# Kernel optimization log

Measured on AMD Instinct MI355X. Metric: run time of the kernel, lower is better.

The kernel has to match this reference:

```python
import jax, jax.numpy as jnp
import numpy as np

B, S, H, NH, DH, FF, R, NE, EI, NT = 8, 1024, 768, 12, 64, 3072, 64, 512, 4096, 8
EPS = 1e-5


def layer_norm(x, g, b):
    m = jnp.mean(x, axis=-1, keepdims=True)
    v = jnp.var(x, axis=-1, keepdims=True)
    return (x - m) * jax.lax.rsqrt(v + EPS) * g + b


def adapter_apply(h, node_idx, edge_idx, types, dw, db, uw, ub, temb):
    """Hypergraph adapter: bottleneck down-proj, node->hyperedge mean gather,
    edge-type embedding, hyperedge->node mean scatter, up-proj. vmapped over batch."""
    def one(hb, nb, eb, tb):
        d = jax.nn.gelu(hb @ dw + db)                                  # [S, R]
        m = d[nb]                                                      # [EI, R] gather node feats per incidence
        ones = jnp.ones((EI,), d.dtype)
        esum = jax.ops.segment_sum(m, eb, num_segments=NE)             # [NE, R]
        ecnt = jax.ops.segment_sum(ones, eb, num_segments=NE)
        e = esum / jnp.maximum(ecnt, 1.0)[:, None] + temb[tb]          # hyperedge feats + type emb
        nsum = jax.ops.segment_sum(e[eb], nb, num_segments=S)          # scatter back to nodes
        ncnt = jax.ops.segment_sum(ones, nb, num_segments=S)
        u = nsum / jnp.maximum(ncnt, 1.0)[:, None]                     # [S, R]
        return u @ uw + ub                                             # [S, H]
    return jax.vmap(one)(h, node_idx, edge_idx, types)


def setup_inputs() -> dict:
    key = jax.random.key(0)
    ks = jax.random.split(key, 24)
    std = 0.02
    p = lambda k, shp: jax.random.normal(k, shp, jnp.float32) * std
    inp = {
        'hidden_states': jax.random.normal(ks[0], (B, S, H), jnp.float32),
        'node_idx': jax.random.randint(ks[1], (B, EI), 0, S, jnp.int32),
        'edge_idx': jax.random.randint(ks[2], (B, EI), 0, NE, jnp.int32),
        'edge_types': jax.random.randint(ks[3], (B, NE), 0, NT, jnp.int32),
        'Wq': p(ks[4], (H, H)), 'bq': jnp.zeros((H,), jnp.float32),
        'Wk': p(ks[5], (H, H)), 'bk': jnp.zeros((H,), jnp.float32),
        'Wv': p(ks[6], (H, H)), 'bv': jnp.zeros((H,), jnp.float32),
        'Wo': p(ks[7], (H, H)), 'bo': jnp.zeros((H,), jnp.float32),
        'ln1_g': jnp.ones((H,), jnp.float32), 'ln1_b': jnp.zeros((H,), jnp.float32),
        'a1_dw': p(ks[8], (H, R)), 'a1_db': jnp.zeros((R,), jnp.float32),
        'a1_uw': p(ks[9], (R, H)), 'a1_ub': jnp.zeros((H,), jnp.float32),
        'a1_temb': p(ks[10], (NT, R)),
        'Wi': p(ks[11], (H, FF)), 'bi': jnp.zeros((FF,), jnp.float32),
        'Wd2': p(ks[12], (FF, H)), 'bd2': jnp.zeros((H,), jnp.float32),
        'ln2_g': jnp.ones((H,), jnp.float32), 'ln2_b': jnp.zeros((H,), jnp.float32),
        'a2_dw': p(ks[13], (H, R)), 'a2_db': jnp.zeros((R,), jnp.float32),
        'a2_uw': p(ks[14], (R, H)), 'a2_ub': jnp.zeros((H,), jnp.float32),
        'a2_temb': p(ks[15], (NT, R)),
    }
    return inp


def reference(hidden_states, node_idx, edge_idx, edge_types,
              Wq, bq, Wk, bk, Wv, bv, Wo, bo, ln1_g, ln1_b,
              a1_dw, a1_db, a1_uw, a1_ub, a1_temb,
              Wi, bi, Wd2, bd2, ln2_g, ln2_b,
              a2_dw, a2_db, a2_uw, a2_ub, a2_temb):
    x = hidden_states
    # --- self attention ---
    q = (x @ Wq + bq).reshape(B, S, NH, DH)
    k = (x @ Wk + bk).reshape(B, S, NH, DH)
    v = (x @ Wv + bv).reshape(B, S, NH, DH)
    scores = jnp.einsum('bqhd,bkhd->bhqk', q, k) / jnp.sqrt(jnp.float32(DH))
    probs = jax.nn.softmax(scores, axis=-1)
    ctx = jnp.einsum('bhqk,bkhd->bqhd', probs, v).reshape(B, S, H)
    attn_dense = ctx @ Wo + bo                                         # dropout = identity (eval)
    # --- hypergraph adapter 1 + residual LN ---
    ad1 = adapter_apply(attn_dense, node_idx, edge_idx, edge_types, a1_dw, a1_db, a1_uw, a1_ub, a1_temb)
    attn_out = layer_norm(attn_dense + ad1 + x, ln1_g, ln1_b)
    # --- FFN ---
    inter = jax.nn.gelu(attn_out @ Wi + bi)
    ff = inter @ Wd2 + bd2
    # --- hypergraph adapter 2 + residual LN ---
    ad2 = adapter_apply(ff, node_idx, edge_idx, edge_types, a2_dw, a2_db, a2_uw, a2_ub, a2_temb)
    layer_output = layer_norm(ff + ad2 + attn_out, ln2_g, ln2_b)
    return layer_output
```

## Files before the change

### kernel.cpp

```cpp
#include <hip/hip_runtime.h>

typedef unsigned short u16;
typedef __attribute__((ext_vector_type(8))) short s16x8;
typedef __attribute__((ext_vector_type(4))) float f32x4;
typedef __attribute__((ext_vector_type(4))) unsigned short u16x4;

#define NB 8
#define SS 1024
#define HH 768
#define NHD 12
#define DHD 64
#define FFD 3072
#define RR 64
#define NEC 512
#define EIC 4096

__device__ __forceinline__ float b2f(u16 u){ return __uint_as_float(((unsigned)u)<<16); }
__device__ __forceinline__ u16 f2b(float f){
  unsigned x = __float_as_uint(f);
  return (u16)((x + 0x7fffu + ((x>>16)&1u)) >> 16);
}
__device__ __forceinline__ float gelu_f(float x){
  return 0.5f*x*(1.0f + tanhf(0.79788456080286535588f*(x + 0.044715f*x*x*x)));
}
__device__ __forceinline__ void xcd_swz(int gx, int gy, int& bx, int& by){
  const int nwg = gx*gy;
  const int flat = by*gx + bx;
  const int qch = nwg >> 3, rch = nwg & 7;
  const int xcd = flat & 7, idx = flat >> 3;
  const int swz = (xcd < rch ? xcd*(qch+1) : rch*(qch+1) + (xcd-rch)*qch) + idx;
  bx = swz % gx; by = swz / gx;
}

__global__ __launch_bounds__(256)
void cvt16(const float* __restrict__ src, u16* __restrict__ dst)
{
  const size_t i = ((size_t)blockIdx.x*256 + threadIdx.x)*8;
  float4 a = *(const float4*)&src[i];
  float4 b = *(const float4*)&src[i+4];
  u16x4 h1; h1.x=f2b(a.x); h1.y=f2b(a.y); h1.z=f2b(a.z); h1.w=f2b(a.w);
  u16x4 h2; h2.x=f2b(b.x); h2.y=f2b(b.y); h2.z=f2b(b.z); h2.w=f2b(b.w);
  *(u16x4*)&dst[i] = h1; *(u16x4*)&dst[i+4] = h2;
}

__global__ __launch_bounds__(256)
void wtrans(const float* __restrict__ src, u16* __restrict__ dst, int R, int C)
{
  __shared__ u16 tile[64][68];
  const int r0 = blockIdx.x*64, c0 = blockIdx.y*64;
  const int t = threadIdx.x;
  const int tr = t >> 4, tc = (t & 15) * 4;
  for (int i = 0; i < 4; i++) {
    int r = tr + i*16;
    float4 v4 = *(const float4*)&src[(size_t)(r0+r)*C + c0 + tc];
    u16x4 h; h.x = f2b(v4.x); h.y = f2b(v4.y); h.z = f2b(v4.z); h.w = f2b(v4.w);
    *(u16x4*)&tile[r][tc] = h;
  }
  __syncthreads();
  for (int i = 0; i < 4; i++) {
    int rr = tr + i*16;
    u16x4 v;
    v.x = tile[tc+0][rr]; v.y = tile[tc+1][rr];
    v.z = tile[tc+2][rr]; v.w = tile[tc+3][rr];
    *(u16x4*)&dst[(size_t)(c0+rr)*R + r0 + tc] = v;
  }
}

__global__ __launch_bounds__(256)
void vtrans(const u16* __restrict__ v, u16* __restrict__ vt, int vs)
{
  __shared__ u16 tile[64][68];
  const int st = blockIdx.x, bh = blockIdx.y;
  const int b = bh / NHD, h = bh - b*NHD;
  const u16* src = v + (size_t)(b*SS + st*64)*vs + h*DHD;
  u16* dst = vt + (size_t)bh*DHD*SS + st*64;
  const int t = threadIdx.x;
  const int tr = t >> 4, tc = (t & 15) * 4;
  for (int i = 0; i < 4; i++) {
    int r = tr + i*16;
    *(u16x4*)&tile[r][tc] = *(const u16x4*)&src[(size_t)r*vs + tc];
  }
  __syncthreads();
  for (int i = 0; i < 4; i++) {
    int rr = tr + i*16;
    u16x4 vv;
    vv.x = tile[tc+0][rr]; vv.y = tile[tc+1][rr];
    vv.z = tile[tc+2][rr]; vv.w = tile[tc+3][rr];
    *(u16x4*)&dst[(size_t)rr*SS + tc] = vv;
  }
}

template<int BM, int BN, int ACT, int OUT>
__global__ __launch_bounds__(256)
void gemm_bt(const u16* __restrict__ A, const u16* __restrict__ Bt,
             const float* __restrict__ bias, float* __restrict__ C32,
             u16* __restrict__ C16, int M, int N, int K)
{
  constexpr int MF = BM/32;
  constexpr int NF = BN/32;
  __shared__ __align__(16) u16 lsA[BM*64];
  __shared__ __align__(16) u16 lsB[BN*64];
  int bx = blockIdx.x, by = blockIdx.y;
  xcd_swz(gridDim.x, gridDim.y, bx, by);
  const int m0 = by*BM, n0 = bx*BN;
  const int t = threadIdx.x, lane = t & 63, w = t >> 6;
  const int wm = w >> 1, wn = w & 1;
  const int l15 = lane & 15, lg = lane >> 4;

  f32x4 acc[MF][NF];
  #pragma unroll
  for (int i = 0; i < MF; i++)
    #pragma unroll
    for (int j = 0; j < NF; j++) acc[i][j] = (f32x4){0.f,0.f,0.f,0.f};

  for (int k0 = 0; k0 < K; k0 += 64) {
    __syncthreads();
    #pragma unroll
    for (int i = 0; i < BM/32; i++) {
      const int p = (w*(BM/32) + i)*64 + lane;
      const int r = p >> 3;
      const int ch = (p & 7) ^ (r & 7);
      __builtin_amdgcn_global_load_lds(
        (const __attribute__((address_space(1))) unsigned*)(A + (size_t)(m0+r)*K + k0 + ch*8),
        (__attribute__((address_space(3))) unsigned*)(lsA + (w*(BM/32)+i)*512),
        16, 0, 0);
    }
    #pragma unroll
    for (int i = 0; i < BN/32; i++) {
      const int p = (w*(BN/32) + i)*64 + lane;
      const int r = p >> 3;
      const int ch = (p & 7) ^ (r & 7);
      __builtin_amdgcn_global_load_lds(
        (const __attribute__((address_space(1))) unsigned*)(Bt + (size_t)(n0+r)*K + k0 + ch*8),
        (__attribute__((address_space(3))) unsigned*)(lsB + (w*(BN/32)+i)*512),
        16, 0, 0);
    }
    __syncthreads();
    #pragma unroll
    for (int kk = 0; kk < 64; kk += 32) {
      const int cb = (kk >> 3) + lg;
      s16x8 af[MF], bfr[NF];
      #pragma unroll
      for (int i = 0; i < MF; i++) {
        const int row = wm*(BM/2) + i*16 + l15;
        af[i] = *(const s16x8*)&lsA[row*64 + ((cb ^ (row & 7)) << 3)];
      }
      #pragma unroll
      for (int j = 0; j < NF; j++) {
        const int row = wn*(BN/2) + j*16 + l15;
        bfr[j] = *(const s16x8*)&lsB[row*64 + ((cb ^ (row & 7)) << 3)];
      }
      #pragma unroll
      for (int i = 0; i < MF; i++)
        #pragma unroll
        for (int j = 0; j < NF; j++)
          acc[i][j] = __builtin_amdgcn_mfma_f32_16x16x32_bf16(af[i], bfr[j], acc[i][j], 0, 0, 0);
    }
  }
  #pragma unroll
  for (int j = 0; j < NF; j++) {
    const int col = n0 + wn*(BN/2) + j*16 + l15;
    const float bv = bias[col];
    #pragma unroll
    for (int i = 0; i < MF; i++) {
      #pragma unroll
      for (int r = 0; r < 4; r++) {
        const int row = m0 + wm*(BM/2) + i*16 + (lg << 2) + r;
        float v = acc[i][j][r] + bv;
        if (ACT == 1) v = gelu_f(v);
        if constexpr (OUT == 0 || OUT == 2) C32[(size_t)row*N + col] = v;
        if constexpr (OUT == 1 || OUT == 2) C16[(size_t)row*N + col] = f2b(v);
      }
    }
  }
}

__global__ __launch_bounds__(256)
void attn_fwd(const u16* __restrict__ q, const u16* __restrict__ k,
              const u16* __restrict__ vt, u16* __restrict__ ctx, int qs)
{
  int bx = blockIdx.x, by = blockIdx.y;
  xcd_swz(gridDim.x, gridDim.y, bx, by);
  const int qt = bx, bh = by;
  const int b = bh / NHD, h = bh - b*NHD;
  __shared__ __align__(16) u16 lsK[64][72];
  __shared__ __align__(16) u16 lsV[64][72];
  __shared__ __align__(16) u16 lsP[4][16][72];
  const int t = threadIdx.x, lane = t & 63, w = t >> 6;
  const int l15 = lane & 15, lg = lane >> 4;

  const int qrow = qt*64 + w*16 + l15;
  const size_t qoff = (size_t)(b*SS + qrow)*qs + h*DHD;
  const s16x8 qf0 = *(const s16x8*)&q[qoff + (lg << 3)];
  const s16x8 qf1 = *(const s16x8*)&q[qoff + 32 + (lg << 3)];

  float m_run[4], l_run[4];
  f32x4 oacc[4];
  #pragma unroll
  for (int r = 0; r < 4; r++) { m_run[r] = -1e30f; l_run[r] = 0.f; }
  #pragma unroll
  for (int j = 0; j < 4; j++) oacc[j] = (f32x4){0.f,0.f,0.f,0.f};

  const u16* kbase = k + (size_t)(b*SS)*qs + h*DHD;
  const u16* vbase = vt + (size_t)bh*DHD*SS;

  for (int kt = 0; kt < SS/64; kt++) {
    __syncthreads();
    for (int c = t; c < 512; c += 256) {
      int r = c >> 3, cc = (c & 7) << 3;
      *(s16x8*)&lsK[r][cc] = *(const s16x8*)&kbase[(size_t)(kt*64 + r)*qs + cc];
    }
    for (int c = t; c < 512; c += 256) {
      int r = c >> 3, cc = (c & 7) << 3;
      *(s16x8*)&lsV[r][cc] = *(const s16x8*)&vbase[(size_t)r*SS + kt*64 + cc];
    }
    __syncthreads();

    f32x4 sc[4];
    #pragma unroll
    for (int nf = 0; nf < 4; nf++) sc[nf] = (f32x4){0.f,0.f,0.f,0.f};
    #pragma unroll
    for (int kk = 0; kk < 2; kk++) {
      const int ko = kk*32 + (lg << 3);
      const s16x8 a = kk ? qf1 : qf0;
      #pragma unroll
      for (int nf = 0; nf < 4; nf++) {
        s16x8 kf = *(const s16x8*)&lsK[nf*16 + l15][ko];
        sc[nf] = __builtin_amdgcn_mfma_f32_16x16x32_bf16(a, kf, sc[nf], 0, 0, 0);
      }
    }
    float alpha[4], pv[4][4];
    #pragma unroll
    for (int r = 0; r < 4; r++) {
      float mx = fmaxf(fmaxf(sc[0][r], sc[1][r]), fmaxf(sc[2][r], sc[3][r])) * 0.125f;
      #pragma unroll
      for (int o = 1; o < 16; o <<= 1) mx = fmaxf(mx, __shfl_xor(mx, o, 64));
      const float nm = fmaxf(m_run[r], mx);
      alpha[r] = __expf(m_run[r] - nm);
      float sum = 0.f;
      #pragma unroll
      for (int nf = 0; nf < 4; nf++) {
        float p = __expf(sc[nf][r]*0.125f - nm);
        pv[nf][r] = p; sum += p;
      }
      #pragma unroll
      for (int o = 1; o < 16; o <<= 1) sum += __shfl_xor(sum, o, 64);
      l_run[r] = l_run[r]*alpha[r] + sum;
      m_run[r] = nm;
    }
    #pragma unroll
    for (int j = 0; j < 4; j++) {
      f32x4 o = oacc[j];
      o[0] *= alpha[0]; o[1] *= alpha[1]; o[2] *= alpha[2]; o[3] *= alpha[3];
      oacc[j] = o;
    }
    #pragma unroll
    for (int nf = 0; nf < 4; nf++)
      #pragma unroll
      for (int r = 0; r < 4; r++)
        lsP[w][(lg << 2) + r][nf*16 + l15] = f2b(pv[nf][r]);
    __syncthreads();
    #pragma unroll
    for (int ks = 0; ks < 2; ks++) {
      const int ko = ks*32 + (lg << 3);
      const s16x8 pf = *(const s16x8*)&lsP[w][l15][ko];
      #pragma unroll
      for (int j = 0; j < 4; j++) {
        s16x8 vf = *(const s16x8*)&lsV[j*16 + l15][ko];
        oacc[j] = __builtin_amdgcn_mfma_f32_16x16x32_bf16(pf, vf, oacc[j], 0, 0, 0);
      }
    }
  }
  #pragma unroll
  for (int j = 0; j < 4; j++)
    #pragma unroll
    for (int r = 0; r < 4; r++) {
      const int row = qt*64 + w*16 + (lg << 2) + r;
      ctx[((size_t)(b*SS + row))*HH + h*DHD + j*16 + l15] = f2b(oacc[j][r] / l_run[r]);
    }
}

__global__ __launch_bounds__(256)
void adp_gather(const float* __restrict__ d, const int* __restrict__ nidx,
                const int* __restrict__ eidx, float* __restrict__ esum,
                float* __restrict__ ecnt)
{
  const int gi = blockIdx.x*4 + (threadIdx.x >> 6);
  const int lane = threadIdx.x & 63;
  const int b = gi >> 12, i = gi & (EIC - 1);
  const int n = nidx[(size_t)b*EIC + i];
  const int e = eidx[(size_t)b*EIC + i];
  const float val = d[((size_t)b*SS + n)*RR + lane];
  atomicAdd(&esum[((size_t)b*NEC + e)*RR + lane], val);
  if (lane == 0) atomicAdd(&ecnt[(size_t)b*NEC + e], 1.0f);
}

__global__ __launch_bounds__(256)
void adp_edge(const float* __restrict__ esum, const float* __restrict__ ecnt,
              const int* __restrict__ types, const float* __restrict__ temb,
              float* __restrict__ e_out)
{
  const int ge = blockIdx.x*4 + (threadIdx.x >> 6);
  const int lane = threadIdx.x & 63;
  const int b = ge >> 9, e = ge & (NEC - 1);
  const float cnt = fmaxf(ecnt[(size_t)b*NEC + e], 1.0f);
  const int ty = types[(size_t)b*NEC + e];
  e_out[((size_t)b*NEC + e)*RR + lane] =
      esum[((size_t)b*NEC + e)*RR + lane]/cnt + temb[(size_t)ty*RR + lane];
}

__global__ __launch_bounds__(256)
void adp_scatter(const float* __restrict__ e_out, const int* __restrict__ nidx,
                 const int* __restrict__ eidx, float* __restrict__ nsum,
                 float* __restrict__ ncnt)
{
  const int gi = blockIdx.x*4 + (threadIdx.x >> 6);
  const int lane = threadIdx.x & 63;
  const int b = gi >> 12, i = gi & (EIC - 1);
  const int n = nidx[(size_t)b*EIC + i];
  const int e = eidx[(size_t)b*EIC + i];
  atomicAdd(&nsum[((size_t)b*SS + n)*RR + lane], e_out[((size_t)b*NEC + e)*RR + lane]);
  if (lane == 0) atomicAdd(&ncnt[(size_t)b*SS + n], 1.0f);
}

__global__ __launch_bounds__(256)
void adp_node(const float* __restrict__ nsum, const float* __restrict__ ncnt,
              u16* __restrict__ u)
{
  const int gn = blockIdx.x*4 + (threadIdx.x >> 6);
  const int lane = threadIdx.x & 63;
  const float cnt = fmaxf(ncnt[gn], 1.0f);
  u[(size_t)gn*RR + lane] = f2b(nsum[(size_t)gn*RR + lane]/cnt);
}

__global__ __launch_bounds__(256)
void ln3(const float* __restrict__ a, const float* __restrict__ bb,
         const float* __restrict__ c, const float* __restrict__ g,
         const float* __restrict__ be, float* __restrict__ out,
         u16* __restrict__ outb)
{
  const int row = blockIdx.x, t = threadIdx.x;
  const size_t base = (size_t)row*HH;
  float v[3]; float s = 0.f, s2 = 0.f;
  #pragma unroll
  for (int i = 0; i < 3; i++) {
    int col = t + i*256;
    float x = a[base+col] + bb[base+col] + c[base+col];
    v[i] = x; s += x; s2 += x*x;
  }
  #pragma unroll
  for (int o = 1; o < 64; o <<= 1) { s += __shfl_xor(s, o, 64); s2 += __shfl_xor(s2, o, 64); }
  __shared__ float red[2][4];
  if ((t & 63) == 0) { red[0][t>>6] = s; red[1][t>>6] = s2; }
  __syncthreads();
  const float S  = red[0][0]+red[0][1]+red[0][2]+red[0][3];
  const float S2 = red[1][0]+red[1][1]+red[1][2]+red[1][3];
  const float mean = S*(1.0f/HH);
  const float var  = S2*(1.0f/HH) - mean*mean;
  const float inv  = rsqrtf(var + 1e-5f);
  #pragma unroll
  for (int i = 0; i < 3; i++) {
    int col = t + i*256;
    const float res = (v[i]-mean)*inv*g[col] + be[col];
    out[base+col] = res;
    if (outb) outb[base+col] = f2b(res);
  }
}

extern "C" void kernel_launch(void* const* d_in, const int* in_sizes, int n_in,
                              void* d_out, int out_size, void* d_ws, size_t ws_size,
                              hipStream_t stream)
{
  (void)in_sizes; (void)n_in; (void)out_size; (void)ws_size;
  const float* x        = (const float*)d_in[0];
  const int* node_idx   = (const int*)d_in[1];
  const int* edge_idx   = (const int*)d_in[2];
  const int* edge_types = (const int*)d_in[3];
  const float* Wq = (const float*)d_in[4];  const float* bq = (const float*)d_in[5];
  const float* Wk = (const float*)d_in[6];  const float* bk = (const float*)d_in[7];
  const float* Wv = (const float*)d_in[8];  const float* bv = (const float*)d_in[9];
  const float* Wo = (const float*)d_in[10]; const float* bo = (const float*)d_in[11];
  const float* ln1_g = (const float*)d_in[12]; const float* ln1_b = (const float*)d_in[13];
  const float* a1_dw = (const float*)d_in[14]; const float* a1_db = (const float*)d_in[15];
  const float* a1_uw = (const float*)d_in[16]; const float* a1_ub = (const float*)d_in[17];
  const float* a1_temb = (const float*)d_in[18];
  const float* Wi  = (const float*)d_in[19]; const float* bi  = (const float*)d_in[20];
  const float* Wd2 = (const float*)d_in[21]; const float* bd2 = (const float*)d_in[22];
  const float* ln2_g = (const float*)d_in[23]; const float* ln2_b = (const float*)d_in[24];
  const float* a2_dw = (const float*)d_in[25]; const float* a2_db = (const float*)d_in[26];
  const float* a2_uw = (const float*)d_in[27]; const float* a2_ub = (const float*)d_in[28];
  const float* a2_temb = (const float*)d_in[29];

  char* ws = (char*)d_ws;
  size_t off = 0;
  auto take = [&](size_t bytes) -> size_t {
    size_t o = off; off += (bytes + 255) & ~(size_t)255; return o;
  };
  const size_t actB2 = (size_t)8192*768*2;
  const size_t actB4 = (size_t)8192*768*4;
  const size_t oWqkvT = take(2304ull*768*2);
  const size_t oWoT   = take(768ull*768*2);
  const size_t oWiT   = take(768ull*3072*2);
  const size_t oWd2T  = take(768ull*3072*2);
  const size_t oA1dwT = take(768ull*64*2);
  const size_t oA1uwT = take(768ull*64*2);
  const size_t oA2dwT = take(768ull*64*2);
  const size_t oA2uwT = take(768ull*64*2);
  const size_t oBqkv  = take(2304ull*4);
  const size_t oXbf  = take(actB2);
  const size_t oQkv  = take((size_t)8192*2304*2);
  const size_t oVt   = take(actB2);
  const size_t oCtx  = take(actB2);
  const size_t oAD   = take(actB4);
  const size_t oAdp  = take(actB4);
  const size_t oAO   = take(actB4);
  const size_t oAOb  = take(actB2);
  const size_t oDb   = take((size_t)8192*64*4);
  const size_t oUb   = take((size_t)8192*64*2);
  const size_t oEsum = take((size_t)8*512*64*4);
  const size_t oEcnt = take((size_t)8*512*4);
  const size_t oNsum = take((size_t)8*1024*64*4);
  const size_t oNcnt = take((size_t)8*1024*4);
  const size_t oEbuf = take((size_t)8*512*64*4);
  const size_t oInter = oQkv;
  const size_t oFF    = oAD;
  const size_t oFFb   = oCtx;
  const size_t oADb   = oXbf;
  const size_t zeroBytes = oEbuf - oEsum;

  u16* WqkvT = (u16*)(ws+oWqkvT); u16* WoT = (u16*)(ws+oWoT);
  u16* WiT = (u16*)(ws+oWiT);     u16* Wd2T = (u16*)(ws+oWd2T);
  u16* A1dwT = (u16*)(ws+oA1dwT); u16* A1uwT = (u16*)(ws+oA1uwT);
  u16* A2dwT = (u16*)(ws+oA2dwT); u16* A2uwT = (u16*)(ws+oA2uwT);
  float* bias_qkv = (float*)(ws+oBqkv);
  u16* xbf = (u16*)(ws+oXbf);
  u16* qkv = (u16*)(ws+oQkv);
  u16* vtb = (u16*)(ws+oVt);  u16* ctx = (u16*)(ws+oCtx);
  float* attn_dense = (float*)(ws+oAD); u16* attn_dense_bf = (u16*)(ws+oADb);
  float* adb = (float*)(ws+oAdp);
  float* attn_out = (float*)(ws+oAO);   u16* attn_out_bf = (u16*)(ws+oAOb);
  float* dbuf = (float*)(ws+oDb);       u16* ubuf = (u16*)(ws+oUb);
  float* esum = (float*)(ws+oEsum); float* ecnt = (float*)(ws+oEcnt);
  float* nsum = (float*)(ws+oNsum); float* ncnt = (float*)(ws+oNcnt);
  float* ebuf = (float*)(ws+oEbuf);
  u16* inter = (u16*)(ws+oInter);
  float* ffb = (float*)(ws+oFF);  u16* ffb_bf = (u16*)(ws+oFFb);

  const dim3 blk(256);
  wtrans<<<dim3(12,12), blk, 0, stream>>>(Wq,  WqkvT,            768, 768);
  wtrans<<<dim3(12,12), blk, 0, stream>>>(Wk,  WqkvT + 768*768,  768, 768);
  wtrans<<<dim3(12,12), blk, 0, stream>>>(Wv,  WqkvT + 2*768*768,768, 768);
  wtrans<<<dim3(12,12), blk, 0, stream>>>(Wo,  WoT,  768, 768);
  wtrans<<<dim3(12,48), blk, 0, stream>>>(Wi,  WiT,  768, 3072);
  wtrans<<<dim3(48,12), blk, 0, stream>>>(Wd2, Wd2T, 3072, 768);
  wtrans<<<dim3(12,1),  blk, 0, stream>>>(a1_dw, A1dwT, 768, 64);
  wtrans<<<dim3(1,12),  blk, 0, stream>>>(a1_uw, A1uwT, 64, 768);
  wtrans<<<dim3(12,1),  blk, 0, stream>>>(a2_dw, A2dwT, 768, 64);
  wtrans<<<dim3(1,12),  blk, 0, stream>>>(a2_uw, A2uwT, 64, 768);
  hipMemcpyAsync(bias_qkv,        bq, 768*4, hipMemcpyDeviceToDevice, stream);
  hipMemcpyAsync(bias_qkv + 768,  bk, 768*4, hipMemcpyDeviceToDevice, stream);
  hipMemcpyAsync(bias_qkv + 1536, bv, 768*4, hipMemcpyDeviceToDevice, stream);
  cvt16<<<3072, blk, 0, stream>>>(x, xbf);
  gemm_bt<64,128,0,1><<<dim3(18,128), blk, 0, stream>>>(xbf, WqkvT, bias_qkv, nullptr, qkv, 8192, 2304, 768);
  vtrans<<<dim3(16,96), blk, 0, stream>>>(qkv + 1536, vtb, 2304);
  attn_fwd<<<dim3(16,96), blk, 0, stream>>>(qkv, qkv + 768, vtb, ctx, 2304);
  gemm_bt<64,128,0,2><<<dim3(6,128), blk, 0, stream>>>(ctx, WoT, bo, attn_dense, attn_dense_bf, 8192, 768, 768);
  gemm_bt<64,64,1,0><<<dim3(1,128), blk, 0, stream>>>(attn_dense_bf, A1dwT, a1_db, dbuf, nullptr, 8192, 64, 768);
  hipMemsetAsync(ws + oEsum, 0, zeroBytes, stream);
  adp_gather<<<8192, blk, 0, stream>>>(dbuf, node_idx, edge_idx, esum, ecnt);
  adp_edge<<<1024, blk, 0, stream>>>(esum, ecnt, edge_types, a1_temb, ebuf);
  adp_scatter<<<8192, blk, 0, stream>>>(ebuf, node_idx, edge_idx, nsum, ncnt);
  adp_node<<<2048, blk, 0, stream>>>(nsum, ncnt, ubuf);
  gemm_bt<64,128,0,0><<<dim3(6,128), blk, 0, stream>>>(ubuf, A1uwT, a1_ub, adb, nullptr, 8192, 768, 64);
  ln3<<<8192, blk, 0, stream>>>(attn_dense, adb, x, ln1_g, ln1_b, attn_out, attn_out_bf);
  gemm_bt<64,128,1,1><<<dim3(24,128), blk, 0, stream>>>(attn_out_bf, WiT, bi, nullptr, inter, 8192, 3072, 768);
  gemm_bt<64,128,0,2><<<dim3(6,128), blk, 0, stream>>>(inter, Wd2T, bd2, ffb, ffb_bf, 8192, 768, 3072);
  gemm_bt<64,64,1,0><<<dim3(1,128), blk, 0, stream>>>(ffb_bf, A2dwT, a2_db, dbuf, nullptr, 8192, 64, 768);
  hipMemsetAsync(ws + oEsum, 0, zeroBytes, stream);
  adp_gather<<<8192, blk, 0, stream>>>(dbuf, node_idx, edge_idx, esum, ecnt);
  adp_edge<<<1024, blk, 0, stream>>>(esum, ecnt, edge_types, a2_temb, ebuf);
  adp_scatter<<<8192, blk, 0, stream>>>(ebuf, node_idx, edge_idx, nsum, ncnt);
  adp_node<<<2048, blk, 0, stream>>>(nsum, ncnt, ubuf);
  gemm_bt<64,128,0,0><<<dim3(6,128), blk, 0, stream>>>(ubuf, A2uwT, a2_ub, adb, nullptr, 8192, 768, 64);
  ln3<<<8192, blk, 0, stream>>>(ffb, adb, attn_out, ln2_g, ln2_b, (float*)d_out, nullptr);
}
```

Before: 629.1 us.

## Transpose QK^T MFMA for in-lane softmax with lazy max rescaling in attention

Swaps the MFMA operands so each lane holds one query column's scores. The row max and row sum then need only two cross-lane shuffles instead of four per row, and the running max and sum become scalars per lane. Rescaling of the output accumulator is skipped unless a wave's max grows by more than 8, since the softmax stays exact when the same stale max is used throughout. It also writes P to shared memory as vectorised 4-wide stores, drops the block barrier before the PV step because the P buffer is private to each wave, and replaces the final divide with a reciprocal multiply. The cost is extra shuffles to hand alpha and 1/l to the output layout, and unnormalised values up to about e^8 stored in bf16.

```diff
diff --git a/kernel.cpp b/kernel.cpp
--- a/kernel.cpp
+++ b/kernel.cpp
@@ -194,10 +194,8 @@
   const s16x8 qf0 = *(const s16x8*)&q[qoff + (lg << 3)];
   const s16x8 qf1 = *(const s16x8*)&q[qoff + 32 + (lg << 3)];
 
-  float m_run[4], l_run[4];
+  float m_run = -1e30f, l_run = 0.f;
   f32x4 oacc[4];
-  #pragma unroll
-  for (int r = 0; r < 4; r++) { m_run[r] = -1e30f; l_run[r] = 0.f; }
   #pragma unroll
   for (int j = 0; j < 4; j++) oacc[j] = (f32x4){0.f,0.f,0.f,0.f};
 
@@ -218,48 +216,54 @@
 
     f32x4 sc[4];
     #pragma unroll
-    for (int nf = 0; nf < 4; nf++) sc[nf] = (f32x4){0.f,0.f,0.f,0.f};
+    for (int mf = 0; mf < 4; mf++) sc[mf] = (f32x4){0.f,0.f,0.f,0.f};
     #pragma unroll
     for (int kk = 0; kk < 2; kk++) {
       const int ko = kk*32 + (lg << 3);
-      const s16x8 a = kk ? qf1 : qf0;
-      #pragma unroll
-      for (int nf = 0; nf < 4; nf++) {
-        s16x8 kf = *(const s16x8*)&lsK[nf*16 + l15][ko];
-        sc[nf] = __builtin_amdgcn_mfma_f32_16x16x32_bf16(a, kf, sc[nf], 0, 0, 0);
-      }
-    }
-    float alpha[4], pv[4][4];
-    #pragma unroll
-    for (int r = 0; r < 4; r++) {
-      float mx = fmaxf(fmaxf(sc[0][r], sc[1][r]), fmaxf(sc[2][r], sc[3][r])) * 0.125f;
-      #pragma unroll
-      for (int o = 1; o < 16; o <<= 1) mx = fmaxf(mx, __shfl_xor(mx, o, 64));
-      const float nm = fmaxf(m_run[r], mx);
-      alpha[r] = __expf(m_run[r] - nm);
-      float sum = 0.f;
-      #pragma unroll
-      for (int nf = 0; nf < 4; nf++) {
-        float p = __expf(sc[nf][r]*0.125f - nm);
-        pv[nf][r] = p; sum += p;
-      }
-      #pragma unroll
-      for (int o = 1; o < 16; o <<= 1) sum += __shfl_xor(sum, o, 64);
-      l_run[r] = l_run[r]*alpha[r] + sum;
-      m_run[r] = nm;
-    }
-    #pragma unroll
-    for (int j = 0; j < 4; j++) {
-      f32x4 o = oacc[j];
-      o[0] *= alpha[0]; o[1] *= alpha[1]; o[2] *= alpha[2]; o[3] *= alpha[3];
-      oacc[j] = o;
-    }
-    #pragma unroll
-    for (int nf = 0; nf < 4; nf++)
-      #pragma unroll
-      for (int r = 0; r < 4; r++)
-        lsP[w][(lg << 2) + r][nf*16 + l15] = f2b(pv[nf][r]);
-    __syncthreads();
+      const s16x8 qv = kk ? qf1 : qf0;
+      #pragma unroll
+      for (int mf = 0; mf < 4; mf++) {
+        s16x8 kf = *(const s16x8*)&lsK[mf*16 + l15][ko];
+        sc[mf] = __builtin_amdgcn_mfma_f32_16x16x32_bf16(kf, qv, sc[mf], 0, 0, 0);
+      }
+    }
+    float pmax = sc[0][0];
+    #pragma unroll
+    for (int mf = 0; mf < 4; mf++)
+      #pragma unroll
+      for (int r = 0; r < 4; r++) pmax = fmaxf(pmax, sc[mf][r]);
+    pmax *= 0.125f;
+    pmax = fmaxf(pmax, __shfl_xor(pmax, 16, 64));
+    pmax = fmaxf(pmax, __shfl_xor(pmax, 32, 64));
+    const bool need = !__all(pmax - m_run <= 8.0f);
+    const float nm = need ? fmaxf(m_run, pmax) : m_run;
+    float sum = 0.f;
+    #pragma unroll
+    for (int mf = 0; mf < 4; mf++) {
+      u16x4 ph;
+      #pragma unroll
+      for (int r = 0; r < 4; r++) {
+        const float p = __expf(sc[mf][r]*0.125f - nm);
+        sum += p;
+        ph[r] = f2b(p);
+      }
+      *(u16x4*)&lsP[w][l15][mf*16 + (lg << 2)] = ph;
+    }
+    sum += __shfl_xor(sum, 16, 64);
+    sum += __shfl_xor(sum, 32, 64);
+    if (need) {
+      const float alpha = __expf(m_run - nm);
+      l_run = l_run*alpha + sum;
+      m_run = nm;
+      #pragma unroll
+      for (int r = 0; r < 4; r++) {
+        const float ar = __shfl(alpha, (lg << 2) + r, 64);
+        #pragma unroll
+        for (int j = 0; j < 4; j++) oacc[j][r] *= ar;
+      }
+    } else {
+      l_run += sum;
+    }
     #pragma unroll
     for (int ks = 0; ks < 2; ks++) {
       const int ko = ks*32 + (lg << 3);
@@ -271,13 +275,16 @@
       }
     }
   }
-  #pragma unroll
-  for (int j = 0; j < 4; j++)
-    #pragma unroll
-    for (int r = 0; r < 4; r++) {
+  const float linv = 1.f / l_run;
+  #pragma unroll
+  for (int r = 0; r < 4; r++) {
+    const float lr = __shfl(linv, (lg << 2) + r, 64);
+    #pragma unroll
+    for (int j = 0; j < 4; j++) {
       const int row = qt*64 + w*16 + (lg << 2) + r;
-      ctx[((size_t)(b*SS + row))*HH + h*DHD + j*16 + l15] = f2b(oacc[j][r] / l_run[r]);
-    }
+      ctx[((size_t)(b*SS + row))*HH + h*DHD + j*16 + l15] = f2b(oacc[j][r] * lr);
+    }
+  }
 }
 
 __global__ __launch_bounds__(256)
```

Measured after the change: 584.0 us. -7.2%, faster.
